# Optimization experiments

Hardware: AMD Instinct MI355X
Metric: run time of the kernel (lower is better)

The kernel has to match this reference:

```python
import jax, jax.numpy as jnp
import numpy as np
import math

C = 1.0
IN_FEATURES = 512
SCALE = 1.0 / math.sqrt(IN_FEATURES)  # 1/sqrt(input_size) * lr_mul, lr_mul=1
LR_MUL = 1.0
GAIN = math.sqrt(2.0)
EPS = 1e-5       # clamp epsilon used by hyptorch-style pmath
PROJ_EPS = 1e-3  # boundary epsilon for project()


def _norm(x):
    return jnp.linalg.norm(x, axis=-1, keepdims=True)


def _artanh(x):
    return jnp.arctanh(jnp.clip(x, -1.0 + EPS, 1.0 - EPS))


def _project(x, c):
    sqrt_c = c ** 0.5
    norm = jnp.maximum(_norm(x), EPS)
    maxnorm = (1.0 - PROJ_EPS) / sqrt_c
    return jnp.where(norm > maxnorm, x / norm * maxnorm, x)


def _expmap0(u, c):
    sqrt_c = c ** 0.5
    u_norm = jnp.maximum(_norm(u), EPS)
    return jnp.tanh(sqrt_c * u_norm) * u / (sqrt_c * u_norm)


def _mobius_add(x, y, c):
    x2 = jnp.sum(x * x, axis=-1, keepdims=True)
    y2 = jnp.sum(y * y, axis=-1, keepdims=True)
    xy = jnp.sum(x * y, axis=-1, keepdims=True)
    num = (1.0 + 2.0 * c * xy + c * y2) * x + (1.0 - c * x2) * y
    denom = 1.0 + 2.0 * c * xy + c * c * x2 * y2
    return num / (denom + EPS)


def _mobius_matvec(m, x, c):
    # m: [out, in], x: [N, in]
    sqrt_c = c ** 0.5
    x_norm = jnp.maximum(_norm(x), EPS)
    mx = x @ m.T  # [N, out]
    mx_norm = jnp.maximum(_norm(mx), EPS)
    res = jnp.tanh(mx_norm / x_norm * _artanh(sqrt_c * x_norm)) * mx / (mx_norm * sqrt_c)
    zero_row = jnp.all(mx == 0, axis=-1, keepdims=True)
    return jnp.where(zero_row, jnp.zeros_like(res), res)


def _mobius_scalar_mult(x, r, c):
    sqrt_c = c ** 0.5
    x_norm = jnp.maximum(_norm(x), EPS)
    return jnp.tanh(r * _artanh(sqrt_c * x_norm)) * x / (x_norm * sqrt_c)


def setup_inputs() -> dict:
    key = jax.random.key(0)
    k1, k2, k3 = jax.random.split(key, 3)
    N, D_IN, D_OUT = 131072, 512, 512
    # scale x so points lie well inside the unit Poincare ball (norm ~ 0.45)
    x = jax.random.normal(k1, (N, D_IN), dtype=jnp.float32) * 0.02
    weight = jax.random.normal(k2, (D_OUT, D_IN), dtype=jnp.float32)
    bias = jax.random.normal(k3, (D_OUT,), dtype=jnp.float32) * 0.01
    return {"x": x, "weight": weight, "bias": bias}


def reference(x, weight, bias):
    c = C
    mv = _mobius_matvec(weight * SCALE, x, c)
    b = _expmap0(bias * LR_MUL, c)
    out = _project(_mobius_add(mv, b[None, :], c), c)
    out = jax.nn.leaky_relu(out, 0.2)
    out = _mobius_scalar_mult(out, GAIN, c)
    return out
```

## Files before the change

### kernel.cpp

```cpp
#include <hip/hip_runtime.h>
#include <math.h>

#define EPSV 1e-5f
#define SCALE_W 0.0441941738241592f
#define GAIN_R 1.4142135623730951f

typedef __attribute__((ext_vector_type(8))) short bf16x8;
typedef __attribute__((ext_vector_type(4))) float f32x4;
typedef __attribute__((ext_vector_type(4))) unsigned int u32x4;

static __device__ __forceinline__ unsigned short f2bf(float f) {
  union { float f; unsigned int u; } v; v.f = f;
  unsigned int r = v.u + 0x7FFFu + ((v.u >> 16) & 1u);
  return (unsigned short)(r >> 16);
}

static __device__ __forceinline__ unsigned int cvtpk(float lo, float hi) {
  unsigned int r;
  asm("v_cvt_pk_bf16_f32 %0, %1, %2" : "=v"(r) : "v"(lo), "v"(hi));
  return r;
}

#define GLD_LDS16(gsrc, ldst)                                                                      \
  __builtin_amdgcn_global_load_lds((const __attribute__((address_space(1))) unsigned int*)(gsrc),  \
                                   (__attribute__((address_space(3))) unsigned int*)(ldst), 16, 0, 0)

#define LBAR() do {                                          \
  asm volatile("s_waitcnt lgkmcnt(0)" ::: "memory");         \
  __builtin_amdgcn_sched_barrier(0);                         \
  __builtin_amdgcn_s_barrier();                              \
  __builtin_amdgcn_sched_barrier(0);                         \
} while (0)

#define VMCNT(N) do {                                        \
  asm volatile("s_waitcnt vmcnt(" #N ")" ::: "memory");      \
  __builtin_amdgcn_sched_barrier(0);                         \
} while (0)

__global__ void bias_expmap_k(const float* __restrict__ bias, float* __restrict__ bexp,
                              float* __restrict__ y2out) {
  __shared__ float part[8];
  int t = threadIdx.x;
  float bv = bias[t];
  float s = bv * bv;
  s += __shfl_xor(s, 1);  s += __shfl_xor(s, 2);  s += __shfl_xor(s, 4);
  s += __shfl_xor(s, 8);  s += __shfl_xor(s, 16); s += __shfl_xor(s, 32);
  if ((t & 63) == 0) part[t >> 6] = s;
  __syncthreads();
  float tot = 0.f;
#pragma unroll
  for (int i = 0; i < 8; ++i) tot += part[i];
  float un = fmaxf(sqrtf(tot), EPSV);
  float th = tanhf(un);
  bexp[t] = th * bv / un;
  if (t == 0) *y2out = th * th;
}

__global__ void pack_weight_k(const float* __restrict__ w, unsigned short* __restrict__ wsB) {
  int e = blockIdx.x * 256 + threadIdx.x;
  int o = e >> 9;
  int k = e & 511;
  int ks = k >> 5, kk = k & 31;
  int lgr = kk >> 3, j = kk & 7;
  int colhi = o >> 4, l15 = o & 15;
  int dst = ((ks * 32 + colhi) * 64 + lgr * 16 + l15) * 8 + j;
  wsB[dst] = f2bf(w[e] * SCALE_W);
}

#define RB 80
#define ABUF 5120
#define BOFF 10240
#define BBUF 32768
#define SCR 75776
#define SMEMSZ 80896

__global__ __launch_bounds__(256, 2)
void hyp_main_k(const float* __restrict__ x, const unsigned short* __restrict__ wsB,
                const float* __restrict__ bexp, const float* __restrict__ y2p,
                float* __restrict__ out, int tilesPerBlk) {
  extern __shared__ char smem[];
  const int tid  = threadIdx.x;
  const int lane = tid & 63;
  const int wave = tid >> 6;
  const int l15  = lane & 15;
  const int lgr  = lane >> 4;
  const int srow = tid >> 2;
  const int sq   = tid & 3;

  float* xn2      = (float*)(smem + SCR);
  float* pS2      = (float*)(smem + SCR + 256);
  float* pSB      = (float*)(smem + SCR + 1280);
  float* g12      = (float*)(smem + SCR + 2304);
  float* bexp_lds = (float*)(smem + SCR + 2816);
  float* y2l      = (float*)(smem + SCR + 4864);

  f32x4 acc[4][8];
#pragma unroll
  for (int mf = 0; mf < 4; ++mf)
#pragma unroll
    for (int nf = 0; nf < 8; ++nf) acc[mf][nf] = f32x4{0.f, 0.f, 0.f, 0.f};

  const long base = (long)blockIdx.x * tilesPerBlk;
  const int U = tilesPerBlk * 16;
  const float* xrow = x + (size_t)(base * 64 + srow) * 512 + sq * 8;
  float xss = 0.f;
  f32x4 ring[2][2];

  {
    float2 bc = *(const float2*)(bexp + tid * 2);
    ring[0][0] = *(const f32x4*)(xrow);
    ring[0][1] = *(const f32x4*)(xrow + 4);
    ring[1][0] = *(const f32x4*)(xrow + 32);
    ring[1][1] = *(const f32x4*)(xrow + 36);
    float y2v = *y2p;
    VMCNT(0);
    *(float2*)(bexp_lds + tid * 2) = bc;
    if (tid == 0) *y2l = y2v;
    f32x4 a = ring[0][0], b = ring[0][1];
    xss += a[0]*a[0] + a[1]*a[1] + a[2]*a[2] + a[3]*a[3];
    xss += b[0]*b[0] + b[1]*b[1] + b[2]*b[2] + b[3]*b[3];
    u32x4 pk;
    pk[0] = cvtpk(a[0], a[1]); pk[1] = cvtpk(a[2], a[3]);
    pk[2] = cvtpk(b[0], b[1]); pk[3] = cvtpk(b[2], b[3]);
    *(u32x4*)(smem + srow * RB + sq * 16) = pk;
#pragma unroll
    for (int i = 0; i < 8; ++i)
      GLD_LDS16((const char*)wsB + (wave * 8 + i) * 1024 + lane * 16,
                smem + BOFF + (wave * 8 + i) * 1024);
  }
  LBAR();

#pragma unroll 2
  for (int t = 0; t < U; ++t) {
    const int cur = t & 1, nxt = cur ^ 1;
    const bool epi = ((t & 15) == 15);

    {
      int gu = t + 2; if (gu >= U) gu = U - 1;
      const float* p = xrow + (size_t)(gu >> 4) * 32768 + (gu & 15) * 32;
      ring[cur][0] = *(const f32x4*)p;
      ring[cur][1] = *(const f32x4*)(p + 4);
    }
    {
      const char* bs = (const char*)wsB + (size_t)((t + 1) & 15) * 32768;
      char* bd = smem + BOFF + nxt * BBUF;
#pragma unroll
      for (int i = 0; i < 8; ++i)
        GLD_LDS16(bs + (wave * 8 + i) * 1024 + lane * 16, bd + (wave * 8 + i) * 1024);
    }
    VMCNT(10);

    {
      const char* ab = smem + cur * ABUF + l15 * RB + lgr * 16;
      const char* bb = smem + BOFF + cur * BBUF + (wave * 8) * 1024 + lane * 16;
      bf16x8 xf[4], wf[8];
#pragma unroll
      for (int mf = 0; mf < 4; ++mf) xf[mf] = *(const bf16x8*)(ab + mf * (16 * RB));
#pragma unroll
      for (int nf = 0; nf < 8; ++nf) wf[nf] = *(const bf16x8*)(bb + nf * 1024);
      __builtin_amdgcn_s_setprio(1);
#pragma unroll
      for (int mf = 0; mf < 4; ++mf)
#pragma unroll
        for (int nf = 0; nf < 8; ++nf)
          acc[mf][nf] = __builtin_amdgcn_mfma_f32_16x16x32_bf16(wf[nf], xf[mf], acc[mf][nf], 0, 0, 0);
      __builtin_amdgcn_s_setprio(0);
    }

    if (epi) {
      const long trow = (base + (t >> 4)) * 64;

      float xs = xss;
      xs += __shfl_xor(xs, 1); xs += __shfl_xor(xs, 2);
      if (sq == 0) xn2[srow] = xs;
      xss = 0.f;

      f32x4 bvv[8];
#pragma unroll
      for (int nf = 0; nf < 8; ++nf)
        bvv[nf] = *(const f32x4*)(bexp_lds + wave * 128 + nf * 16 + lgr * 4);

      float s2[4], sb[4];
#pragma unroll
      for (int mf = 0; mf < 4; ++mf) {
        s2[mf] = 0.f; sb[mf] = 0.f;
#pragma unroll
        for (int nf = 0; nf < 8; ++nf)
#pragma unroll
          for (int j = 0; j < 4; ++j) {
            float v = acc[mf][nf][j];
            s2[mf] += v * v;
            sb[mf] += v * bvv[nf][j];
          }
        s2[mf] += __shfl_xor(s2[mf], 16); s2[mf] += __shfl_xor(s2[mf], 32);
        sb[mf] += __shfl_xor(sb[mf], 16); sb[mf] += __shfl_xor(sb[mf], 32);
      }
      if (lane < 16) {
#pragma unroll
        for (int mf = 0; mf < 4; ++mf) {
          pS2[(mf * 16 + l15) * 4 + wave] = s2[mf];
          pSB[(mf * 16 + l15) * 4 + wave] = sb[mf];
        }
      }
      LBAR();

      if (tid < 64) {
        int r = tid;
        float S2 = 0.f, SB = 0.f;
#pragma unroll
        for (int i = 0; i < 4; ++i) { S2 += pS2[r * 4 + i]; SB += pSB[r * 4 + i]; }
        float y2s = *y2l;
        float xn  = fmaxf(sqrtf(xn2[r]), EPSV);
        float mxn = fmaxf(sqrtf(S2), EPSV);
        float f = tanhf((mxn / xn) * atanhf(fminf(xn, 1.f - EPSV))) / mxn;
        float xy = f * SB;
        float x2 = f * f * S2;
        float den = 1.f + 2.f * xy + x2 * y2s + EPSV;
        float g1 = (1.f + 2.f * xy + y2s) * f / den;
        float g2 = (1.f - x2) / den;
        float n1sq = g1 * g1 * S2 + 2.f * g1 * g2 * SB + g2 * g2 * y2s;
        float n1 = fmaxf(sqrtf(fmaxf(n1sq, 0.f)), EPSV);
        if (n1 > 0.999f) { float sc = 0.999f / n1; g1 *= sc; g2 *= sc; }
        g12[r * 2] = g1; g12[r * 2 + 1] = g2;
      }
      LBAR();

      float n2p[4];
#pragma unroll
      for (int mf = 0; mf < 4; ++mf) {
        float g1 = g12[(mf * 16 + l15) * 2], g2 = g12[(mf * 16 + l15) * 2 + 1];
        n2p[mf] = 0.f;
#pragma unroll
        for (int nf = 0; nf < 8; ++nf)
#pragma unroll
          for (int j = 0; j < 4; ++j) {
            float v = g1 * acc[mf][nf][j] + g2 * bvv[nf][j];
            v = v > 0.f ? v : 0.2f * v;
            acc[mf][nf][j] = v;
            n2p[mf] += v * v;
          }
        n2p[mf] += __shfl_xor(n2p[mf], 16); n2p[mf] += __shfl_xor(n2p[mf], 32);
      }
      if (lane < 16) {
#pragma unroll
        for (int mf = 0; mf < 4; ++mf) pS2[(mf * 16 + l15) * 4 + wave] = n2p[mf];
      }
      LBAR();

      if (tid < 64) {
        int r = tid;
        float sn = 0.f;
#pragma unroll
        for (int i = 0; i < 4; ++i) sn += pS2[r * 4 + i];
        float n2 = fmaxf(sqrtf(sn), EPSV);
        xn2[r] = tanhf(GAIN_R * atanhf(fminf(n2, 1.f - EPSV))) / n2;
      }
      LBAR();

#pragma unroll
      for (int mf = 0; mf < 4; ++mf) {
        float tm = xn2[mf * 16 + l15];
#pragma unroll
        for (int nf = 0; nf < 8; ++nf) {
          f32x4 o = acc[mf][nf];
          o[0] *= tm; o[1] *= tm; o[2] *= tm; o[3] *= tm;
          *(f32x4*)(out + (size_t)(trow + mf * 16 + l15) * 512 +
                    wave * 128 + nf * 16 + lgr * 4) = o;
          acc[mf][nf] = f32x4{0.f, 0.f, 0.f, 0.f};
        }
      }
    }

    {
      f32x4 a = ring[nxt][0], b = ring[nxt][1];
      xss += a[0]*a[0] + a[1]*a[1] + a[2]*a[2] + a[3]*a[3];
      xss += b[0]*b[0] + b[1]*b[1] + b[2]*b[2] + b[3]*b[3];
      u32x4 pk;
      pk[0] = cvtpk(a[0], a[1]); pk[1] = cvtpk(a[2], a[3]);
      pk[2] = cvtpk(b[0], b[1]); pk[3] = cvtpk(b[2], b[3]);
      *(u32x4*)(smem + nxt * ABUF + srow * RB + sq * 16) = pk;
    }
    LBAR();
  }
}

extern "C" void kernel_launch(void* const* d_in, const int* in_sizes, int n_in,
                              void* d_out, int out_size, void* d_ws, size_t ws_size,
                              hipStream_t stream) {
  const float* x    = (const float*)d_in[0];
  const float* w    = (const float*)d_in[1];
  const float* bias = (const float*)d_in[2];
  float* out = (float*)d_out;

  unsigned short* wsB = (unsigned short*)d_ws;
  float* bexp = (float*)((char*)d_ws + 524288);
  float* y2p  = (float*)((char*)d_ws + 524288 + 2048);

  bias_expmap_k<<<dim3(1), dim3(512), 0, stream>>>(bias, bexp, y2p);
  pack_weight_k<<<dim3(1024), dim3(256), 0, stream>>>(w, wsB);

  const int nrows  = in_sizes[0] / 512;
  const int ntiles = nrows / 64;
  const int nblk   = 512;
  const int tpb    = ntiles / nblk;
  hyp_main_k<<<dim3(nblk), dim3(256), SMEMSZ, stream>>>(x, wsB, bexp, y2p, out, tpb);
}
```

Measured before the change: 191.2 us.

## Remove per-step block barriers by giving each wave private operand buffers

The main loop is rebuilt so each wave loads its own X fragments straight from global memory into registers. It converts them to bf16 and accumulates the row norms in registers. Each wave also streams its own weight slice into a private LDS double buffer, so the block-wide barrier on every K step goes away and barriers remain only in the epilogue. The cost is that all four waves now read the same X rows, multiplying X traffic through the caches. The bias vector in LDS is also first read with no barrier after it is written.

```diff
diff --git a/kernel.cpp b/kernel.cpp
--- a/kernel.cpp
+++ b/kernel.cpp
@@ -67,32 +67,26 @@
   wsB[dst] = f2bf(w[e] * SCALE_W);
 }
 
-#define RB 80
-#define ABUF 5120
-#define BOFF 10240
-#define BBUF 32768
-#define SCR 75776
-#define SMEMSZ 80896
+#define SCR 65536
+#define SMEMSZ 70400
 
 __global__ __launch_bounds__(256, 2)
-void hyp_main_k(const float* __restrict__ x, const unsigned short* __restrict__ wsB,
-                const float* __restrict__ bexp, const float* __restrict__ y2p,
-                float* __restrict__ out, int tilesPerBlk) {
+void hyp_nobar_k(const float* __restrict__ x, const unsigned short* __restrict__ wsB,
+                 const float* __restrict__ bexp, const float* __restrict__ y2p,
+                 float* __restrict__ out, int tilesPerBlk) {
   extern __shared__ char smem[];
   const int tid  = threadIdx.x;
   const int lane = tid & 63;
   const int wave = tid >> 6;
   const int l15  = lane & 15;
   const int lgr  = lane >> 4;
-  const int srow = tid >> 2;
-  const int sq   = tid & 3;
-
+
+  char* bbase = smem + wave * 16384;
   float* xn2      = (float*)(smem + SCR);
   float* pS2      = (float*)(smem + SCR + 256);
   float* pSB      = (float*)(smem + SCR + 1280);
   float* g12      = (float*)(smem + SCR + 2304);
   float* bexp_lds = (float*)(smem + SCR + 2816);
-  float* y2l      = (float*)(smem + SCR + 4864);
 
   f32x4 acc[4][8];
 #pragma unroll
@@ -102,33 +96,27 @@
 
   const long base = (long)blockIdx.x * tilesPerBlk;
   const int U = tilesPerBlk * 16;
-  const float* xrow = x + (size_t)(base * 64 + srow) * 512 + sq * 8;
-  float xss = 0.f;
-  f32x4 ring[2][2];
+  const float* xlp = x + ((size_t)base * 64 + l15) * 512 + lgr * 8;
+
+  const float y2v = *y2p;
 
   {
     float2 bc = *(const float2*)(bexp + tid * 2);
-    ring[0][0] = *(const f32x4*)(xrow);
-    ring[0][1] = *(const f32x4*)(xrow + 4);
-    ring[1][0] = *(const f32x4*)(xrow + 32);
-    ring[1][1] = *(const f32x4*)(xrow + 36);
-    float y2v = *y2p;
-    VMCNT(0);
     *(float2*)(bexp_lds + tid * 2) = bc;
-    if (tid == 0) *y2l = y2v;
-    f32x4 a = ring[0][0], b = ring[0][1];
-    xss += a[0]*a[0] + a[1]*a[1] + a[2]*a[2] + a[3]*a[3];
-    xss += b[0]*b[0] + b[1]*b[1] + b[2]*b[2] + b[3]*b[3];
-    u32x4 pk;
-    pk[0] = cvtpk(a[0], a[1]); pk[1] = cvtpk(a[2], a[3]);
-    pk[2] = cvtpk(b[0], b[1]); pk[3] = cvtpk(b[2], b[3]);
-    *(u32x4*)(smem + srow * RB + sq * 16) = pk;
-#pragma unroll
-    for (int i = 0; i < 8; ++i)
-      GLD_LDS16((const char*)wsB + (wave * 8 + i) * 1024 + lane * 16,
-                smem + BOFF + (wave * 8 + i) * 1024);
   }
-  LBAR();
+
+  float xss[4] = {0.f, 0.f, 0.f, 0.f};
+  f32x4 xb[2][4][2];
+
+#pragma unroll
+  for (int i = 0; i < 8; ++i)
+    GLD_LDS16((const char*)wsB + (wave * 8 + i) * 1024 + lane * 16, bbase + i * 1024);
+#pragma unroll
+  for (int mf = 0; mf < 4; ++mf) {
+    const float* p = xlp + mf * 8192;
+    xb[0][mf][0] = *(const f32x4*)p;
+    xb[0][mf][1] = *(const f32x4*)(p + 4);
+  }
 
 #pragma unroll 2
   for (int t = 0; t < U; ++t) {
@@ -136,44 +124,68 @@
     const bool epi = ((t & 15) == 15);
 
     {
-      int gu = t + 2; if (gu >= U) gu = U - 1;
-      const float* p = xrow + (size_t)(gu >> 4) * 32768 + (gu & 15) * 32;
-      ring[cur][0] = *(const f32x4*)p;
-      ring[cur][1] = *(const f32x4*)(p + 4);
+      const char* bs = (const char*)wsB + (size_t)((t + 1) & 15) * 32768;
+      char* bd = bbase + nxt * 8192;
+#pragma unroll
+      for (int i = 0; i < 8; ++i)
+        GLD_LDS16(bs + (wave * 8 + i) * 1024 + lane * 16, bd + i * 1024);
     }
     {
-      const char* bs = (const char*)wsB + (size_t)((t + 1) & 15) * 32768;
-      char* bd = smem + BOFF + nxt * BBUF;
-#pragma unroll
-      for (int i = 0; i < 8; ++i)
-        GLD_LDS16(bs + (wave * 8 + i) * 1024 + lane * 16, bd + (wave * 8 + i) * 1024);
-    }
-    VMCNT(10);
+      int gu = t + 1; if (gu >= U) gu = U - 1;
+      const float* p0 = xlp + (size_t)(gu >> 4) * 32768 + (gu & 15) * 32;
+#pragma unroll
+      for (int mf = 0; mf < 4; ++mf) {
+        xb[nxt][mf][0] = *(const f32x4*)(p0 + mf * 8192);
+        xb[nxt][mf][1] = *(const f32x4*)(p0 + mf * 8192 + 4);
+      }
+    }
+    VMCNT(16);
+
+    u32x4 xf[4];
+#pragma unroll
+    for (int mf = 0; mf < 4; ++mf) {
+      f32x4 a = xb[cur][mf][0], b = xb[cur][mf][1];
+      xss[mf] += a[0]*a[0] + a[1]*a[1] + a[2]*a[2] + a[3]*a[3]
+               + b[0]*b[0] + b[1]*b[1] + b[2]*b[2] + b[3]*b[3];
+      xf[mf][0] = cvtpk(a[0], a[1]); xf[mf][1] = cvtpk(a[2], a[3]);
+      xf[mf][2] = cvtpk(b[0], b[1]); xf[mf][3] = cvtpk(b[2], b[3]);
+    }
 
     {
-      const char* ab = smem + cur * ABUF + l15 * RB + lgr * 16;
-      const char* bb = smem + BOFF + cur * BBUF + (wave * 8) * 1024 + lane * 16;
-      bf16x8 xf[4], wf[8];
-#pragma unroll
-      for (int mf = 0; mf < 4; ++mf) xf[mf] = *(const bf16x8*)(ab + mf * (16 * RB));
-#pragma unroll
-      for (int nf = 0; nf < 8; ++nf) wf[nf] = *(const bf16x8*)(bb + nf * 1024);
+      const char* bb = bbase + cur * 8192 + lane * 16;
+      bf16x8 wf[4];
       __builtin_amdgcn_s_setprio(1);
 #pragma unroll
-      for (int mf = 0; mf < 4; ++mf)
-#pragma unroll
-        for (int nf = 0; nf < 8; ++nf)
-          acc[mf][nf] = __builtin_amdgcn_mfma_f32_16x16x32_bf16(wf[nf], xf[mf], acc[mf][nf], 0, 0, 0);
+      for (int nf = 0; nf < 4; ++nf) wf[nf] = *(const bf16x8*)(bb + nf * 1024);
+#pragma unroll
+      for (int mf = 0; mf < 4; ++mf) {
+        const bf16x8 xv = __builtin_bit_cast(bf16x8, xf[mf]);
+#pragma unroll
+        for (int nf = 0; nf < 4; ++nf)
+          acc[mf][nf] = __builtin_amdgcn_mfma_f32_16x16x32_bf16(wf[nf], xv, acc[mf][nf], 0, 0, 0);
+      }
+#pragma unroll
+      for (int nf = 0; nf < 4; ++nf) wf[nf] = *(const bf16x8*)(bb + (4 + nf) * 1024);
+#pragma unroll
+      for (int mf = 0; mf < 4; ++mf) {
+        const bf16x8 xv = __builtin_bit_cast(bf16x8, xf[mf]);
+#pragma unroll
+        for (int nf = 0; nf < 4; ++nf)
+          acc[mf][4 + nf] = __builtin_amdgcn_mfma_f32_16x16x32_bf16(wf[nf], xv, acc[mf][4 + nf], 0, 0, 0);
+      }
       __builtin_amdgcn_s_setprio(0);
     }
 
     if (epi) {
       const long trow = (base + (t >> 4)) * 64;
 
-      float xs = xss;
-      xs += __shfl_xor(xs, 1); xs += __shfl_xor(xs, 2);
-      if (sq == 0) xn2[srow] = xs;
-      xss = 0.f;
+#pragma unroll
+      for (int mf = 0; mf < 4; ++mf) {
+        float v = xss[mf];
+        v += __shfl_xor(v, 16); v += __shfl_xor(v, 32);
+        if (lane < 16) xn2[mf * 16 + l15] = v;
+        xss[mf] = 0.f;
+      }
 
       f32x4 bvv[8];
 #pragma unroll
@@ -209,16 +221,15 @@
         float S2 = 0.f, SB = 0.f;
 #pragma unroll
         for (int i = 0; i < 4; ++i) { S2 += pS2[r * 4 + i]; SB += pSB[r * 4 + i]; }
-        float y2s = *y2l;
         float xn  = fmaxf(sqrtf(xn2[r]), EPSV);
         float mxn = fmaxf(sqrtf(S2), EPSV);
         float f = tanhf((mxn / xn) * atanhf(fminf(xn, 1.f - EPSV))) / mxn;
         float xy = f * SB;
         float x2 = f * f * S2;
-        float den = 1.f + 2.f * xy + x2 * y2s + EPSV;
-        float g1 = (1.f + 2.f * xy + y2s) * f / den;
+        float den = 1.f + 2.f * xy + x2 * y2v + EPSV;
+        float g1 = (1.f + 2.f * xy + y2v) * f / den;
         float g2 = (1.f - x2) / den;
-        float n1sq = g1 * g1 * S2 + 2.f * g1 * g2 * SB + g2 * g2 * y2s;
+        float n1sq = g1 * g1 * S2 + 2.f * g1 * g2 * SB + g2 * g2 * y2v;
         float n1 = fmaxf(sqrtf(fmaxf(n1sq, 0.f)), EPSV);
         if (n1 > 0.999f) { float sc = 0.999f / n1; g1 *= sc; g2 *= sc; }
         g12[r * 2] = g1; g12[r * 2 + 1] = g2;
@@ -269,18 +280,8 @@
           acc[mf][nf] = f32x4{0.f, 0.f, 0.f, 0.f};
         }
       }
-    }
-
-    {
-      f32x4 a = ring[nxt][0], b = ring[nxt][1];
-      xss += a[0]*a[0] + a[1]*a[1] + a[2]*a[2] + a[3]*a[3];
-      xss += b[0]*b[0] + b[1]*b[1] + b[2]*b[2] + b[3]*b[3];
-      u32x4 pk;
-      pk[0] = cvtpk(a[0], a[1]); pk[1] = cvtpk(a[2], a[3]);
-      pk[2] = cvtpk(b[0], b[1]); pk[3] = cvtpk(b[2], b[3]);
-      *(u32x4*)(smem + nxt * ABUF + srow * RB + sq * 16) = pk;
-    }
-    LBAR();
+      LBAR();
+    }
   }
 }
 
@@ -303,5 +304,5 @@
   const int ntiles = nrows / 64;
   const int nblk   = 512;
   const int tpb    = ntiles / nblk;
-  hyp_main_k<<<dim3(nblk), dim3(256), SMEMSZ, stream>>>(x, wsB, bexp, y2p, out, tpb);
-}
+  hyp_nobar_k<<<dim3(nblk), dim3(256), SMEMSZ, stream>>>(x, wsB, bexp, y2p, out, tpb);
+}
```

Result: slower. 559.1 us (+192.4%).
